# Optimization experiments

Measured on AMD Instinct MI355X. Metric: run time of the kernel, lower is better.

## Reference

```python
import jax, jax.numpy as jnp
import numpy as np

E = 8       # num experts
D = 768     # embed_dim
H = 12      # num heads
F = 3072    # expert hidden = 4*D
TOPK = 2


def setup_inputs() -> dict:
    key = jax.random.key(0)
    ks = jax.random.split(key, 8)
    B, S = 4, 1024
    s = lambda d: 1.0 / np.sqrt(d)
    return {
        "x": jax.random.normal(ks[0], (B, S, D), jnp.float32),
        "w_qkv": jax.random.normal(ks[1], (D, 3 * D), jnp.float32) * s(D),
        "b_qkv": jnp.zeros((3 * D,), jnp.float32),
        "w_o": jax.random.normal(ks[2], (D, D), jnp.float32) * s(D),
        "b_o": jnp.zeros((D,), jnp.float32),
        "w_router": jax.random.normal(ks[3], (D, E), jnp.float32) * s(D),
        "w1": jax.random.normal(ks[4], (E, D, F), jnp.float32) * s(D),
        "b1": jnp.zeros((E, F), jnp.float32),
        "w2": jax.random.normal(ks[5], (E, F, D), jnp.float32) * s(F),
        "b2": jnp.zeros((E, D), jnp.float32),
    }


def reference(x, w_qkv, b_qkv, w_o, b_o, w_router, w1, b1, w2, b2):
    B, S, Dm = x.shape
    hd = Dm // H
    # --- multi-head self-attention ---
    qkv = x @ w_qkv + b_qkv                                  # [B,S,3D]
    q, k, v = jnp.split(qkv, 3, axis=-1)
    resh = lambda t: t.reshape(B, S, H, hd).transpose(0, 2, 1, 3)  # [B,H,S,hd]
    q, k, v = resh(q), resh(k), resh(v)
    scores = jnp.einsum('bhqd,bhkd->bhqk', q, k) / np.sqrt(hd).astype(np.float32)
    attn = jax.nn.softmax(scores, axis=-1)
    ctx = jnp.einsum('bhqk,bhkd->bhqd', attn, v)
    ctx = ctx.transpose(0, 2, 1, 3).reshape(B, S, Dm)
    y = ctx @ w_o + b_o                                      # [B,S,D]
    # --- top-k MoE feed-forward ---
    t = y.reshape(B * S, Dm)                                 # [T,D]
    logits = t @ w_router                                    # [T,E]
    probs = jax.nn.softmax(logits, axis=-1)
    topv, topi = jax.lax.top_k(probs, TOPK)                  # [T,K]
    topw = topv / jnp.sum(topv, axis=-1, keepdims=True)      # renormalized gates
    T = t.shape[0]
    wfull = jnp.zeros_like(probs).at[jnp.arange(T)[:, None], topi].set(topw)  # [T,E]
    # dense all-expert compute, weighted combine (faithful to routed math)
    h = jax.nn.gelu(jnp.einsum('td,edf->etf', t, w1) + b1[:, None, :])  # [E,T,F]
    oe = jnp.einsum('etf,efd->etd', h, w2) + b2[:, None, :]              # [E,T,D]
    out = jnp.einsum('te,etd->td', wfull, oe).reshape(B, S, Dm)
    diagnostics = probs  # router probabilities as diagnostics
    return (out, diagnostics)
```

## Files before the change

kernel.cpp:

```cpp
#include <hip/hip_runtime.h>
#include <hip/hip_bf16.h>
#include <cstdint>
#include <cmath>

#define T_TOK 4096
#define DIM   768
#define HEADS 12
#define HD    64
#define NEXP  8
#define FDIM  3072

typedef __attribute__((ext_vector_type(8))) short short8v;
typedef __attribute__((ext_vector_type(4))) float float4v;

__device__ __forceinline__ float gelu_tanh(float x) {
  float u = 0.7978845608028654f * (x + 0.044715f * x * x * x);
  return 0.5f * x * (1.0f + tanhf(u));
}

__device__ __forceinline__ short f2bf(float x) {
  __hip_bfloat16 h = __float2bfloat16(x);
  return *reinterpret_cast<short*>(&h);
}

__device__ __forceinline__ void gld16(void* lds, const void* g) {
  __builtin_amdgcn_global_load_lds(
      (__attribute__((address_space(1))) void*)(uintptr_t)g,
      (__attribute__((address_space(3))) void*)(uint32_t)(uintptr_t)lds,
      16, 0, 0);
}

template<int TBM, int TBN>
__global__ __launch_bounds__(256) void gemm_f32(
    const float* __restrict__ A, const float* __restrict__ W,
    const float* __restrict__ bias, float* __restrict__ C,
    int M, int N, int K)
{
  constexpr int MM = TBM / 16;
  constexpr int MN = TBN / 16;
  constexpr int ALOAD = TBM * 16 / 256;
  constexpr int BLOAD = TBN * 16 / 256;
  __shared__ float As[16][TBM + 4];
  __shared__ float Bs[16][TBN + 4];
  const int bm = blockIdx.y * TBM;
  const int bn = blockIdx.x * TBN;
  const int tid = threadIdx.x;
  const int tr = tid >> 4;
  const int tc = tid & 15;

  float acc[MM][MN] = {};

  for (int k0 = 0; k0 < K; k0 += 16) {
    #pragma unroll
    for (int i = 0; i < ALOAD; i++) {
      int idx = tid + i * 256;
      int m  = idx >> 4;
      int kk = idx & 15;
      As[kk][m] = A[(size_t)(bm + m) * K + k0 + kk];
    }
    #pragma unroll
    for (int i = 0; i < BLOAD; i++) {
      int idx = tid + i * 256;
      int kk = idx / TBN;
      int n  = idx % TBN;
      Bs[kk][n] = W[(size_t)(k0 + kk) * N + bn + n];
    }
    __syncthreads();
    #pragma unroll
    for (int kk = 0; kk < 16; kk++) {
      float a[MM], b[MN];
      #pragma unroll
      for (int u4 = 0; u4 < MM / 4; u4++) {
        float4 t = *(const float4*)&As[kk][tr * MM + u4 * 4];
        a[u4*4+0]=t.x; a[u4*4+1]=t.y; a[u4*4+2]=t.z; a[u4*4+3]=t.w;
      }
      #pragma unroll
      for (int v4 = 0; v4 < MN / 4; v4++) {
        float4 t = *(const float4*)&Bs[kk][tc * MN + v4 * 4];
        b[v4*4+0]=t.x; b[v4*4+1]=t.y; b[v4*4+2]=t.z; b[v4*4+3]=t.w;
      }
      #pragma unroll
      for (int u = 0; u < MM; u++)
        #pragma unroll
        for (int v = 0; v < MN; v++)
          acc[u][v] = fmaf(a[u], b[v], acc[u][v]);
    }
    __syncthreads();
  }

  #pragma unroll
  for (int u = 0; u < MM; u++) {
    int row = bm + tr * MM + u;
    #pragma unroll
    for (int v4 = 0; v4 < MN / 4; v4++) {
      int col = bn + tc * MN + v4 * 4;
      float4 o;
      o.x = acc[u][v4*4+0] + bias[col+0];
      o.y = acc[u][v4*4+1] + bias[col+1];
      o.z = acc[u][v4*4+2] + bias[col+2];
      o.w = acc[u][v4*4+3] + bias[col+3];
      *(float4*)&C[(size_t)row * N + col] = o;
    }
  }
}

__global__ __launch_bounds__(256) void transpose_bf16(
    const float* __restrict__ W, short* __restrict__ WT, int K, int N)
{
  __shared__ float t[32][33];
  const size_t mat = (size_t)K * N;
  const float* Wp = W + blockIdx.z * mat;
  short* WTp = WT + blockIdx.z * mat;
  int n0 = blockIdx.x * 32, k0 = blockIdx.y * 32;
  int tx = threadIdx.x, ty = threadIdx.y;
  #pragma unroll
  for (int i = 0; i < 4; i++)
    t[ty + i * 8][tx] = Wp[(size_t)(k0 + ty + i * 8) * N + n0 + tx];
  __syncthreads();
  #pragma unroll
  for (int i = 0; i < 4; i++)
    WTp[(size_t)(n0 + ty + i * 8) * K + k0 + tx] = f2bf(t[tx][ty + i * 8]);
}

__global__ __launch_bounds__(256) void y2bf_kernel(
    const float* __restrict__ y, short* __restrict__ ybf)
{
  int g = blockIdx.x * 256 + threadIdx.x;
  float4 v = *(const float4*)&y[(size_t)g * 4];
  short4 s = make_short4(f2bf(v.x), f2bf(v.y), f2bf(v.z), f2bf(v.w));
  *(short4*)&ybf[(size_t)g * 4] = s;
}

__global__ __launch_bounds__(256) void moe_up(
    const short* __restrict__ ybf, const short* __restrict__ WT,
    const float* __restrict__ bias, short* __restrict__ hbuf,
    const int* __restrict__ offsets, const int* __restrict__ perm)
{
  const int e = blockIdx.z;
  const int start = offsets[e];
  const int M = offsets[e + 1] - start;
  const int bm = blockIdx.y * 128;
  if (bm >= M) return;
  const int bn = blockIdx.x * 128;

  __shared__ short As[4][128][8];
  __shared__ short Bs[4][128][8];
  __shared__ int   perm_s[128];

  const int tid  = threadIdx.x;
  const int lane = tid & 63;
  const int wave = tid >> 6;
  const int wm = wave >> 1, wn = wave & 1;
  const int lr = lane & 15;
  const int kb = lane >> 4;

  const short* WTe = WT + (size_t)e * ((size_t)FDIM * DIM);
  const float* be  = bias + (size_t)e * FDIM;

  if (tid < 128) {
    int rr = bm + tid;
    perm_s[tid] = (rr < M) ? perm[start + rr] : perm[start];
  }
  __syncthreads();

  const short* asrc0 = ybf + (size_t)perm_s[lane] * DIM + wave * 8;
  const short* asrc1 = ybf + (size_t)perm_s[64 + lane] * DIM + wave * 8;
  const short* bsrc0 = WTe + (size_t)(bn + lane) * DIM + wave * 8;
  const short* bsrc1 = WTe + (size_t)(bn + 64 + lane) * DIM + wave * 8;
  short* adst0 = &As[wave][0][0];
  short* adst1 = &As[wave][64][0];
  short* bdst0 = &Bs[wave][0][0];
  short* bdst1 = &Bs[wave][64][0];

  float4v acc[4][4] = {};

  for (int k0 = 0; k0 < DIM; k0 += 32) {
    __syncthreads();
    gld16(adst0, asrc0 + k0);
    gld16(adst1, asrc1 + k0);
    gld16(bdst0, bsrc0 + k0);
    gld16(bdst1, bsrc1 + k0);
    __syncthreads();

    short8v af[4], bfv[4];
    #pragma unroll
    for (int mi = 0; mi < 4; mi++)
      af[mi] = *(const short8v*)&As[kb][wm * 64 + mi * 16 + lr][0];
    #pragma unroll
    for (int ni = 0; ni < 4; ni++)
      bfv[ni] = *(const short8v*)&Bs[kb][wn * 64 + ni * 16 + lr][0];
    #pragma unroll
    for (int mi = 0; mi < 4; mi++)
      #pragma unroll
      for (int ni = 0; ni < 4; ni++)
        acc[mi][ni] = __builtin_amdgcn_mfma_f32_16x16x32_bf16(
            af[mi], bfv[ni], acc[mi][ni], 0, 0, 0);
  }

  #pragma unroll
  for (int ni = 0; ni < 4; ni++) {
    int col = bn + wn * 64 + ni * 16 + lr;
    float b = be[col];
    #pragma unroll
    for (int mi = 0; mi < 4; mi++) {
      int lrow0 = wm * 64 + mi * 16 + kb * 4;
      #pragma unroll
      for (int r = 0; r < 4; r++) {
        int rr = bm + lrow0 + r;
        if (rr < M)
          hbuf[(size_t)(start + rr) * FDIM + col] = f2bf(gelu_tanh(acc[mi][ni][r] + b));
      }
    }
  }
}

__global__ __launch_bounds__(256) void moe_down(
    const short* __restrict__ hbuf, const short* __restrict__ WT,
    const float* __restrict__ bias, float* __restrict__ oe,
    const int* __restrict__ offsets)
{
  const int e = blockIdx.z;
  const int start = offsets[e];
  const int M = offsets[e + 1] - start;
  const int bm = blockIdx.y * 64;
  if (bm >= M) return;
  const int bn = blockIdx.x * 128;

  __shared__ short As[4][64][8];
  __shared__ short Bs[4][128][8];

  const int tid  = threadIdx.x;
  const int lane = tid & 63;
  const int wave = tid >> 6;
  const int lr   = lane & 15;
  const int kb   = lane >> 4;

  const short* WTe = WT + (size_t)e * ((size_t)DIM * FDIM);
  const float* be  = bias + (size_t)e * DIM;

  int arow = bm + lane; if (arow >= M) arow = M - 1;
  const short* asrc  = hbuf + (size_t)(start + arow) * FDIM + wave * 8;
  const short* bsrc0 = WTe + (size_t)(bn + lane) * FDIM + wave * 8;
  const short* bsrc1 = WTe + (size_t)(bn + 64 + lane) * FDIM + wave * 8;
  short* adst  = &As[wave][0][0];
  short* bdst0 = &Bs[wave][0][0];
  short* bdst1 = &Bs[wave][64][0];

  float4v acc[4][2] = {};

  for (int k0 = 0; k0 < FDIM; k0 += 32) {
    __syncthreads();
    gld16(adst,  asrc  + k0);
    gld16(bdst0, bsrc0 + k0);
    gld16(bdst1, bsrc1 + k0);
    __syncthreads();

    short8v af[4], bfv[2];
    #pragma unroll
    for (int mi = 0; mi < 4; mi++)
      af[mi] = *(const short8v*)&As[kb][mi * 16 + lr][0];
    #pragma unroll
    for (int ni = 0; ni < 2; ni++)
      bfv[ni] = *(const short8v*)&Bs[kb][wave * 32 + ni * 16 + lr][0];
    #pragma unroll
    for (int mi = 0; mi < 4; mi++)
      #pragma unroll
      for (int ni = 0; ni < 2; ni++)
        acc[mi][ni] = __builtin_amdgcn_mfma_f32_16x16x32_bf16(
            af[mi], bfv[ni], acc[mi][ni], 0, 0, 0);
  }

  #pragma unroll
  for (int ni = 0; ni < 2; ni++) {
    int col = bn + wave * 32 + ni * 16 + lr;
    float b = be[col];
    #pragma unroll
    for (int mi = 0; mi < 4; mi++) {
      #pragma unroll
      for (int r = 0; r < 4; r++) {
        int rr = bm + mi * 16 + kb * 4 + r;
        if (rr < M)
          oe[(size_t)(start + rr) * DIM + col] = acc[mi][ni][r] + b;
      }
    }
  }
}

__global__ __launch_bounds__(256) void combine_kernel(
    const float* __restrict__ oe, const int* __restrict__ ppos,
    const float* __restrict__ topg, float* __restrict__ out)
{
  int g = blockIdx.x * 256 + threadIdx.x;
  int t = g / 192;
  int c = (g - t * 192) * 4;
  int p0 = ppos[2 * t], p1 = ppos[2 * t + 1];
  float g0 = topg[2 * t], g1 = topg[2 * t + 1];
  float4 a = *(const float4*)&oe[(size_t)p0 * DIM + c];
  float4 b = *(const float4*)&oe[(size_t)p1 * DIM + c];
  float4 o;
  o.x = g0 * a.x + g1 * b.x;
  o.y = g0 * a.y + g1 * b.y;
  o.z = g0 * a.z + g1 * b.z;
  o.w = g0 * a.w + g1 * b.w;
  *(float4*)&out[(size_t)t * DIM + c] = o;
}

__global__ __launch_bounds__(512) void attn_kernel(
    const float* __restrict__ qkv, float* __restrict__ ctx)
{
  const int qt = blockIdx.x;
  const int bh = blockIdx.y;
  const int b = bh / HEADS, h = bh % HEADS;
  const float* base = qkv + (size_t)b * 1024 * (3 * DIM) + h * 64;

  __shared__ float ks[64 * 64];
  __shared__ float vs[64 * 64];
  __shared__ float lred[2][2][32];

  const int tid   = threadIdx.x;
  const int wv    = tid >> 6;
  const int qhalf = wv & 1;
  const int kq    = wv >> 1;
  const int lane  = tid & 63;
  const int grp   = lane >> 2;
  const int sub   = lane & 3;
  const int q0    = qhalf * 32 + grp * 2;
  const int dpart = sub * 16;

  const float qscale = 0.125f * 1.44269504088896f;
  float qA[16], qB[16], accA[16] = {}, accB[16] = {};
  float lA = 0.f, lB = 0.f;

  {
    const float* qpA = base + (size_t)(qt * 64 + q0) * (3 * DIM) + dpart;
    const float* qpB = qpA + 3 * DIM;
    #pragma unroll
    for (int d4 = 0; d4 < 4; d4++) {
      float4 ta = *(const float4*)(qpA + d4 * 4);
      float4 tb = *(const float4*)(qpB + d4 * 4);
      qA[d4*4+0]=ta.x*qscale; qA[d4*4+1]=ta.y*qscale; qA[d4*4+2]=ta.z*qscale; qA[d4*4+3]=ta.w*qscale;
      qB[d4*4+0]=tb.x*qscale; qB[d4*4+1]=tb.y*qscale; qB[d4*4+2]=tb.z*qscale; qB[d4*4+3]=tb.w*qscale;
    }
  }

  for (int kt = 0; kt < 16; kt++) {
    __syncthreads();
    #pragma unroll
    for (int i = 0; i < 2; i++) {
      int idx = tid + i * 512;
      int r = idx >> 4, c4 = idx & 15;
      const float* kp = base + (size_t)(kt * 64 + r) * (3 * DIM) + c4 * 4;
      *(float4*)&ks[r * 64 + c4 * 4] = *(const float4*)(kp + DIM);
      *(float4*)&vs[r * 64 + c4 * 4] = *(const float4*)(kp + 2 * DIM);
    }
    __syncthreads();

    #pragma unroll 2
    for (int jj = 0; jj < 16; jj++) {
      int j = kq * 16 + jj;
      float4 k0v = *(const float4*)&ks[j * 64 + dpart];
      float4 k1v = *(const float4*)&ks[j * 64 + dpart + 4];
      float4 k2v = *(const float4*)&ks[j * 64 + dpart + 8];
      float4 k3v = *(const float4*)&ks[j * 64 + dpart + 12];
      float kr[16] = {k0v.x,k0v.y,k0v.z,k0v.w, k1v.x,k1v.y,k1v.z,k1v.w,
                      k2v.x,k2v.y,k2v.z,k2v.w, k3v.x,k3v.y,k3v.z,k3v.w};
      float sA = 0.f, sB = 0.f;
      #pragma unroll
      for (int d = 0; d < 16; d++) {
        sA = fmaf(qA[d], kr[d], sA);
        sB = fmaf(qB[d], kr[d], sB);
      }
      sA += __shfl_xor(sA, 1);  sB += __shfl_xor(sB, 1);
      sA += __shfl_xor(sA, 2);  sB += __shfl_xor(sB, 2);
      float pA = exp2f(sA);
      float pB = exp2f(sB);
      lA += pA;  lB += pB;
      float4 v0v = *(const float4*)&vs[j * 64 + dpart];
      float4 v1v = *(const float4*)&vs[j * 64 + dpart + 4];
      float4 v2v = *(const float4*)&vs[j * 64 + dpart + 8];
      float4 v3v = *(const float4*)&vs[j * 64 + dpart + 12];
      float vr[16] = {v0v.x,v0v.y,v0v.z,v0v.w, v1v.x,v1v.y,v1v.z,v1v.w,
                      v2v.x,v2v.y,v2v.z,v2v.w, v3v.x,v3v.y,v3v.z,v3v.w};
      #pragma unroll
      for (int d = 0; d < 16; d++) {
        accA[d] = fmaf(pA, vr[d], accA[d]);
        accB[d] = fmaf(pB, vr[d], accB[d]);
      }
    }
  }

  float* regA = ks + qhalf * 2048;
  float* regB = vs + qhalf * 2048;
  const int r0 = (grp * 2) * 64 + dpart;
  const int r1 = r0 + 64;

  __syncthreads();
  if (kq == 2 || kq == 3) {
    float* buf = (kq == 2) ? regA : regB;
    #pragma unroll
    for (int d4 = 0; d4 < 4; d4++) {
      *(float4*)&buf[r0 + d4*4] =
          make_float4(accA[d4*4], accA[d4*4+1], accA[d4*4+2], accA[d4*4+3]);
      *(float4*)&buf[r1 + d4*4] =
          make_float4(accB[d4*4], accB[d4*4+1], accB[d4*4+2], accB[d4*4+3]);
    }
    if (sub == 0) {
      lred[kq - 2][qhalf][grp * 2]     = lA;
      lred[kq - 2][qhalf][grp * 2 + 1] = lB;
    }
  }
  __syncthreads();
  if (kq == 0 || kq == 1) {
    const float* buf = (kq == 0) ? regA : regB;
    #pragma unroll
    for (int d4 = 0; d4 < 4; d4++) {
      float4 a = *(const float4*)&buf[r0 + d4*4];
      float4 c = *(const float4*)&buf[r1 + d4*4];
      accA[d4*4+0] += a.x; accA[d4*4+1] += a.y; accA[d4*4+2] += a.z; accA[d4*4+3] += a.w;
      accB[d4*4+0] += c.x; accB[d4*4+1] += c.y; accB[d4*4+2] += c.z; accB[d4*4+3] += c.w;
    }
    lA += lred[kq][qhalf][grp * 2];
    lB += lred[kq][qhalf][grp * 2 + 1];
  }
  __syncthreads();
  if (kq == 1) {
    #pragma unroll
    for (int d4 = 0; d4 < 4; d4++) {
      *(float4*)&regA[r0 + d4*4] =
          make_float4(accA[d4*4], accA[d4*4+1], accA[d4*4+2], accA[d4*4+3]);
      *(float4*)&regA[r1 + d4*4] =
          make_float4(accB[d4*4], accB[d4*4+1], accB[d4*4+2], accB[d4*4+3]);
    }
    if (sub == 0) {
      lred[0][qhalf][grp * 2]     = lA;
      lred[0][qhalf][grp * 2 + 1] = lB;
    }
  }
  __syncthreads();
  if (kq == 0) {
    #pragma unroll
    for (int d4 = 0; d4 < 4; d4++) {
      float4 a = *(const float4*)&regA[r0 + d4*4];
      float4 c = *(const float4*)&regA[r1 + d4*4];
      accA[d4*4+0] += a.x; accA[d4*4+1] += a.y; accA[d4*4+2] += a.z; accA[d4*4+3] += a.w;
      accB[d4*4+0] += c.x; accB[d4*4+1] += c.y; accB[d4*4+2] += c.z; accB[d4*4+3] += c.w;
    }
    lA += lred[0][qhalf][grp * 2];
    lB += lred[0][qhalf][grp * 2 + 1];
    float invA = 1.f / lA, invB = 1.f / lB;
    float* opA = ctx + ((size_t)b * 1024 + qt * 64 + q0) * DIM + h * 64 + dpart;
    float* opB = opA + DIM;
    #pragma unroll
    for (int d4 = 0; d4 < 4; d4++) {
      float4 oa, ob;
      oa.x = accA[d4*4+0]*invA; oa.y = accA[d4*4+1]*invA;
      oa.z = accA[d4*4+2]*invA; oa.w = accA[d4*4+3]*invA;
      ob.x = accB[d4*4+0]*invB; ob.y = accB[d4*4+1]*invB;
      ob.z = accB[d4*4+2]*invB; ob.w = accB[d4*4+3]*invB;
      *(float4*)(opA + d4 * 4) = oa;
      *(float4*)(opB + d4 * 4) = ob;
    }
  }
}

__global__ __launch_bounds__(256) void router_kernel(
    const float* __restrict__ y, const float* __restrict__ wr,
    float* __restrict__ probs, int* __restrict__ topi,
    float* __restrict__ topg, int* __restrict__ counts)
{
  __shared__ float w[DIM * NEXP];
  const int tid = threadIdx.x;
  for (int i = tid; i < DIM * NEXP; i += 256) w[i] = wr[i];
  __syncthreads();

  const int t = blockIdx.x * 256 + tid;
  const float* yp = y + (size_t)t * DIM;
  float logit[8] = {};
  for (int d = 0; d < DIM; d++) {
    float xv = yp[d];
    #pragma unroll
    for (int e = 0; e < 8; e++) logit[e] = fmaf(xv, w[d * 8 + e], logit[e]);
  }
  float mx = logit[0];
  #pragma unroll
  for (int e = 1; e < 8; e++) mx = fmaxf(mx, logit[e]);
  float p[8], sum = 0.f;
  #pragma unroll
  for (int e = 0; e < 8; e++) { p[e] = __expf(logit[e] - mx); sum += p[e]; }
  float inv = 1.f / sum;
  #pragma unroll
  for (int e = 0; e < 8; e++) { p[e] *= inv; probs[(size_t)t * 8 + e] = p[e]; }

  int i0 = 0;
  #pragma unroll
  for (int e = 1; e < 8; e++) if (p[e] > p[i0]) i0 = e;
  int i1 = (i0 == 0) ? 1 : 0;
  #pragma unroll
  for (int e = 0; e < 8; e++) if (e != i0 && p[e] > p[i1]) i1 = e;
  float g = p[i0] + p[i1];
  topi[2 * t] = i0;  topi[2 * t + 1] = i1;
  topg[2 * t] = p[i0] / g;  topg[2 * t + 1] = p[i1] / g;
  atomicAdd(&counts[i0], 1);
  atomicAdd(&counts[i1], 1);
}

__global__ void init_meta(int* counts) {
  if (threadIdx.x < 8) counts[threadIdx.x] = 0;
}

__global__ void scan_kernel(const int* __restrict__ counts,
                            int* __restrict__ offsets, int* __restrict__ cursors) {
  if (threadIdx.x == 0) {
    int s = 0;
    for (int e = 0; e < 8; e++) { offsets[e] = s; cursors[e] = s; s += counts[e]; }
    offsets[8] = s;
  }
}

__global__ __launch_bounds__(256) void scatter_kernel(
    const int* __restrict__ topi, int* __restrict__ cursors,
    int* __restrict__ perm, int* __restrict__ ppos)
{
  const int t = blockIdx.x * 256 + threadIdx.x;
  #pragma unroll
  for (int s = 0; s < 2; s++) {
    int e = topi[2 * t + s];
    int pos = atomicAdd(&cursors[e], 1);
    perm[pos] = t;
    ppos[2 * t + s] = pos;
  }
}

extern "C" void kernel_launch(void* const* d_in, const int* in_sizes, int n_in,
                              void* d_out, int out_size, void* d_ws, size_t ws_size,
                              hipStream_t stream) {
  const float* x        = (const float*)d_in[0];
  const float* w_qkv    = (const float*)d_in[1];
  const float* b_qkv    = (const float*)d_in[2];
  const float* w_o      = (const float*)d_in[3];
  const float* b_o      = (const float*)d_in[4];
  const float* w_router = (const float*)d_in[5];
  const float* w1       = (const float*)d_in[6];
  const float* b1       = (const float*)d_in[7];
  const float* w2       = (const float*)d_in[8];
  const float* b2       = (const float*)d_in[9];

  float* out   = (float*)d_out;
  float* probs = out + (size_t)T_TOK * DIM;

  char* ws = (char*)d_ws;
  float* qkv  = (float*)ws;
  short* hbuf = (short*)ws;
  short* wT   = (short*)(ws + 50331648);
  float* ctx  = (float*)(ws + 88080384);
  short* ybf  = (short*)(ws + 88080384);
  float* oe   = (float*)(ws + 88080384);
  float* y    = (float*)(ws + 100663296);
  char*  meta = ws + 113246208;
  int*   counts  = (int*)meta;
  int*   cursors = counts + 8;
  int*   offsets = cursors + 8;
  int*   topi    = offsets + 16;
  float* topg    = (float*)(topi + 8192);
  int*   perm    = (int*)(topg + 8192);
  int*   ppos    = perm + 8192;

  init_meta<<<1, 64, 0, stream>>>(counts);

  gemm_f32<128, 64><<<dim3((3 * DIM) / 64, T_TOK / 128), 256, 0, stream>>>(
      x, w_qkv, b_qkv, qkv, T_TOK, 3 * DIM, DIM);

  attn_kernel<<<dim3(16, 48), 512, 0, stream>>>(qkv, ctx);

  gemm_f32<64, 64><<<dim3(DIM / 64, T_TOK / 64), 256, 0, stream>>>(
      ctx, w_o, b_o, y, T_TOK, DIM, DIM);

  router_kernel<<<16, 256, 0, stream>>>(y, w_router, probs, topi, topg, counts);
  scan_kernel<<<1, 64, 0, stream>>>(counts, offsets, cursors);
  scatter_kernel<<<16, 256, 0, stream>>>(topi, cursors, perm, ppos);

  y2bf_kernel<<<(T_TOK * DIM / 4) / 256, 256, 0, stream>>>(y, ybf);

  transpose_bf16<<<dim3(FDIM / 32, DIM / 32, NEXP), dim3(32, 8), 0, stream>>>(
      w1, wT, DIM, FDIM);
  moe_up<<<dim3(FDIM / 128, T_TOK / 128, NEXP), 256, 0, stream>>>(
      ybf, wT, b1, hbuf, offsets, perm);

  transpose_bf16<<<dim3(DIM / 32, FDIM / 32, NEXP), dim3(32, 8), 0, stream>>>(
      w2, wT, FDIM, DIM);
  moe_down<<<dim3(DIM / 128, T_TOK / 64, NEXP), 256, 0, stream>>>(
      hbuf, wT, b2, oe, offsets);

  combine_kernel<<<(T_TOK * DIM / 4) / 256, 256, 0, stream>>>(oe, ppos, topg, out);
}
```

Baseline: 1.080 ms.

## Compact MoE tile grids, vectorize fp32 GEMM loads, fuse bf16 cast into out-proj

The scan kernel now builds a compact list of (expert, row-tile) pairs, so moe_up and moe_down launch only about as many tiles as needed instead of a full per-expert grid where most blocks exit early. The fp32 GEMM loads A and W tiles with float4 global reads. The output-projection GEMM also writes the bf16 copy of y, which removes the separate conversion kernel. In exchange the launch grids are sized to fixed upper bounds (72 and 136 tiles), and the A-tile stores into LDS become transposed scalar writes.

```diff
diff --git a/kernel.cpp b/kernel.cpp
--- a/kernel.cpp
+++ b/kernel.cpp
@@ -30,16 +30,16 @@
       16, 0, 0);
 }
 
-template<int TBM, int TBN>
+template<int TBM, int TBN, bool BFOUT>
 __global__ __launch_bounds__(256) void gemm_f32(
     const float* __restrict__ A, const float* __restrict__ W,
     const float* __restrict__ bias, float* __restrict__ C,
-    int M, int N, int K)
+    short* __restrict__ Cbf, int M, int N, int K)
 {
   constexpr int MM = TBM / 16;
   constexpr int MN = TBN / 16;
-  constexpr int ALOAD = TBM * 16 / 256;
-  constexpr int BLOAD = TBN * 16 / 256;
+  constexpr int AL4 = TBM / 64;
+  constexpr int BL4 = TBN / 64;
   __shared__ float As[16][TBM + 4];
   __shared__ float Bs[16][TBN + 4];
   const int bm = blockIdx.y * TBM;
@@ -52,18 +52,21 @@
 
   for (int k0 = 0; k0 < K; k0 += 16) {
     #pragma unroll
-    for (int i = 0; i < ALOAD; i++) {
-      int idx = tid + i * 256;
-      int m  = idx >> 4;
-      int kk = idx & 15;
-      As[kk][m] = A[(size_t)(bm + m) * K + k0 + kk];
-    }
-    #pragma unroll
-    for (int i = 0; i < BLOAD; i++) {
-      int idx = tid + i * 256;
-      int kk = idx / TBN;
-      int n  = idx % TBN;
-      Bs[kk][n] = W[(size_t)(k0 + kk) * N + bn + n];
+    for (int i = 0; i < AL4; i++) {
+      int fidx = tid + i * 256;
+      int row = fidx >> 2, c4 = fidx & 3;
+      float4 v = *(const float4*)&A[(size_t)(bm + row) * K + k0 + c4 * 4];
+      As[c4 * 4 + 0][row] = v.x;
+      As[c4 * 4 + 1][row] = v.y;
+      As[c4 * 4 + 2][row] = v.z;
+      As[c4 * 4 + 3][row] = v.w;
+    }
+    #pragma unroll
+    for (int i = 0; i < BL4; i++) {
+      int fidx = tid + i * 256;
+      int kk = fidx / (TBN / 4), n4 = fidx % (TBN / 4);
+      *(float4*)&Bs[kk][n4 * 4] =
+          *(const float4*)&W[(size_t)(k0 + kk) * N + bn + n4 * 4];
     }
     __syncthreads();
     #pragma unroll
@@ -100,6 +103,10 @@
       o.z = acc[u][v4*4+2] + bias[col+2];
       o.w = acc[u][v4*4+3] + bias[col+3];
       *(float4*)&C[(size_t)row * N + col] = o;
+      if (BFOUT) {
+        short4 s = make_short4(f2bf(o.x), f2bf(o.y), f2bf(o.z), f2bf(o.w));
+        *(short4*)&Cbf[(size_t)row * N + col] = s;
+      }
     }
   }
 }
@@ -122,26 +129,20 @@
     WTp[(size_t)(n0 + ty + i * 8) * K + k0 + tx] = f2bf(t[tx][ty + i * 8]);
 }
 
-__global__ __launch_bounds__(256) void y2bf_kernel(
-    const float* __restrict__ y, short* __restrict__ ybf)
-{
-  int g = blockIdx.x * 256 + threadIdx.x;
-  float4 v = *(const float4*)&y[(size_t)g * 4];
-  short4 s = make_short4(f2bf(v.x), f2bf(v.y), f2bf(v.z), f2bf(v.w));
-  *(short4*)&ybf[(size_t)g * 4] = s;
-}
-
 __global__ __launch_bounds__(256) void moe_up(
     const short* __restrict__ ybf, const short* __restrict__ WT,
     const float* __restrict__ bias, short* __restrict__ hbuf,
-    const int* __restrict__ offsets, const int* __restrict__ perm)
-{
-  const int e = blockIdx.z;
+    const int* __restrict__ offsets, const int* __restrict__ perm,
+    const int* __restrict__ tmap, const int* __restrict__ tilecnt)
+{
+  const int by = blockIdx.y;
+  if (by >= tilecnt[0]) return;
+  const int info  = tmap[by];
+  const int e     = info >> 16;
   const int start = offsets[e];
-  const int M = offsets[e + 1] - start;
-  const int bm = blockIdx.y * 128;
-  if (bm >= M) return;
-  const int bn = blockIdx.x * 128;
+  const int M     = offsets[e + 1] - start;
+  const int bm    = (info & 0xffff) * 128;
+  const int bn    = blockIdx.x * 128;
 
   __shared__ short As[4][128][8];
   __shared__ short Bs[4][128][8];
@@ -217,14 +218,17 @@
 __global__ __launch_bounds__(256) void moe_down(
     const short* __restrict__ hbuf, const short* __restrict__ WT,
     const float* __restrict__ bias, float* __restrict__ oe,
-    const int* __restrict__ offsets)
-{
-  const int e = blockIdx.z;
+    const int* __restrict__ offsets,
+    const int* __restrict__ tmap, const int* __restrict__ tilecnt)
+{
+  const int by = blockIdx.y;
+  if (by >= tilecnt[1]) return;
+  const int info  = tmap[by];
+  const int e     = info >> 16;
   const int start = offsets[e];
-  const int M = offsets[e + 1] - start;
-  const int bm = blockIdx.y * 64;
-  if (bm >= M) return;
-  const int bn = blockIdx.x * 128;
+  const int M     = offsets[e + 1] - start;
+  const int bm    = (info & 0xffff) * 64;
+  const int bn    = blockIdx.x * 128;
 
   __shared__ short As[4][64][8];
   __shared__ short Bs[4][128][8];
@@ -509,11 +513,21 @@
 }
 
 __global__ void scan_kernel(const int* __restrict__ counts,
-                            int* __restrict__ offsets, int* __restrict__ cursors) {
+                            int* __restrict__ offsets, int* __restrict__ cursors,
+                            int* __restrict__ tmap_up, int* __restrict__ tmap_dn,
+                            int* __restrict__ tilecnt) {
   if (threadIdx.x == 0) {
     int s = 0;
     for (int e = 0; e < 8; e++) { offsets[e] = s; cursors[e] = s; s += counts[e]; }
     offsets[8] = s;
+    int tu = 0, td = 0;
+    for (int e = 0; e < 8; e++) {
+      int m = counts[e];
+      for (int t = 0; t * 128 < m; t++) tmap_up[tu++] = (e << 16) | t;
+      for (int t = 0; t * 64  < m; t++) tmap_dn[td++] = (e << 16) | t;
+    }
+    tilecnt[0] = tu;
+    tilecnt[1] = td;
   }
 }
 
@@ -553,10 +567,10 @@
   short* hbuf = (short*)ws;
   short* wT   = (short*)(ws + 50331648);
   float* ctx  = (float*)(ws + 88080384);
-  short* ybf  = (short*)(ws + 88080384);
   float* oe   = (float*)(ws + 88080384);
   float* y    = (float*)(ws + 100663296);
-  char*  meta = ws + 113246208;
+  short* ybf  = (short*)(ws + 113246208);
+  char*  meta = ws + 119537664;
   int*   counts  = (int*)meta;
   int*   cursors = counts + 8;
   int*   offsets = cursors + 8;
@@ -564,32 +578,34 @@
   float* topg    = (float*)(topi + 8192);
   int*   perm    = (int*)(topg + 8192);
   int*   ppos    = perm + 8192;
+  int*   tmap_up = ppos + 8192;
+  int*   tmap_dn = tmap_up + 80;
+  int*   tilecnt = tmap_dn + 144;
 
   init_meta<<<1, 64, 0, stream>>>(counts);
 
-  gemm_f32<128, 64><<<dim3((3 * DIM) / 64, T_TOK / 128), 256, 0, stream>>>(
-      x, w_qkv, b_qkv, qkv, T_TOK, 3 * DIM, DIM);
+  gemm_f32<128, 64, false><<<dim3((3 * DIM) / 64, T_TOK / 128), 256, 0, stream>>>(
+      x, w_qkv, b_qkv, qkv, nullptr, T_TOK, 3 * DIM, DIM);
 
   attn_kernel<<<dim3(16, 48), 512, 0, stream>>>(qkv, ctx);
 
-  gemm_f32<64, 64><<<dim3(DIM / 64, T_TOK / 64), 256, 0, stream>>>(
-      ctx, w_o, b_o, y, T_TOK, DIM, DIM);
+  gemm_f32<64, 64, true><<<dim3(DIM / 64, T_TOK / 64), 256, 0, stream>>>(
+      ctx, w_o, b_o, y, ybf, T_TOK, DIM, DIM);
 
   router_kernel<<<16, 256, 0, stream>>>(y, w_router, probs, topi, topg, counts);
-  scan_kernel<<<1, 64, 0, stream>>>(counts, offsets, cursors);
+  scan_kernel<<<1, 64, 0, stream>>>(counts, offsets, cursors,
+                                    tmap_up, tmap_dn, tilecnt);
   scatter_kernel<<<16, 256, 0, stream>>>(topi, cursors, perm, ppos);
-
-  y2bf_kernel<<<(T_TOK * DIM / 4) / 256, 256, 0, stream>>>(y, ybf);
 
   transpose_bf16<<<dim3(FDIM / 32, DIM / 32, NEXP), dim3(32, 8), 0, stream>>>(
       w1, wT, DIM, FDIM);
-  moe_up<<<dim3(FDIM / 128, T_TOK / 128, NEXP), 256, 0, stream>>>(
-      ybf, wT, b1, hbuf, offsets, perm);
+  moe_up<<<dim3(FDIM / 128, 72), 256, 0, stream>>>(
+      ybf, wT, b1, hbuf, offsets, perm, tmap_up, tilecnt);
 
   transpose_bf16<<<dim3(DIM / 32, FDIM / 32, NEXP), dim3(32, 8), 0, stream>>>(
       w2, wT, FDIM, DIM);
-  moe_down<<<dim3(DIM / 128, T_TOK / 64, NEXP), 256, 0, stream>>>(
-      hbuf, wT, b2, oe, offsets);
+  moe_down<<<dim3(DIM / 128, 136), 256, 0, stream>>>(
+      hbuf, wT, b2, oe, offsets, tmap_dn, tilecnt);
 
   combine_kernel<<<(T_TOK * DIM / 4) / 256, 256, 0, stream>>>(oe, ppos, topg, out);
 }
```

Measured after the change: 1.029 ms. 4.7% less time.
